# Performance work log

Hardware: AMD Instinct MI355X
Metric: run time of the kernel (lower is better)

The kernel has to match this reference:

```python
import jax, jax.numpy as jnp
import numpy as np

B, N, K = 8, 2048, 20
NC = 50
EPS = 1e-5
SLOPE = 0.2


def _knn(xt, k):
    # xt: [B, N, C]; negative squared euclidean distance, top-k (includes self)
    xx = jnp.sum(xt * xt, axis=-1)                      # [B, N]
    inner = jnp.einsum('bnc,bmc->bnm', xt, xt)          # [B, N, N]
    dist = 2.0 * inner - xx[:, :, None] - xx[:, None, :]
    return jax.lax.top_k(dist, k)[1]                    # [B, N, k] int32


def _edge_conv(xt, w, g, b, k):
    # xt: [B, N, C]; w: [O, 2C]; BatchNorm2d over (B, N, k) per out-channel.
    idx = _knn(xt, k)
    nbr = xt[jnp.arange(B)[:, None, None], idx]          # [B, N, k, C]
    ctr = jnp.broadcast_to(xt[:, :, None, :], nbr.shape)
    edge = jnp.concatenate([nbr - ctr, ctr], axis=-1)    # [B, N, k, 2C]
    h = jnp.einsum('bnkc,oc->bnko', edge, w)             # 1x1 conv, no bias
    mu = jnp.mean(h, axis=(0, 1, 2))
    var = jnp.var(h, axis=(0, 1, 2))
    h = (h - mu) / jnp.sqrt(var + EPS) * g + b
    h = jnp.where(h > 0, h, SLOPE * h)                   # LeakyReLU(0.2)
    return jnp.max(h, axis=2)                            # max over k -> [B, N, O]


def _bn1d(y, g, b):
    mu = jnp.mean(y, axis=0)
    var = jnp.var(y, axis=0)
    return (y - mu) / jnp.sqrt(var + EPS) * g + b


def setup_inputs() -> dict:
    key = jax.random.key(0)
    ks = jax.random.split(key, 20)

    def rn(k, shape, scale):
        return jax.random.normal(k, shape, dtype=jnp.float32) * scale

    d = {
        'x': rn(ks[0], (B * N, 3), 1.0),
        'pos': rn(ks[1], (B * N, 3), 1.0),
        'batch': jnp.repeat(jnp.arange(B, dtype=jnp.int64), N),
        'edge_index': jax.random.randint(ks[2], (2, B * N), 0, B * N, dtype=jnp.int64),
        # EdgeConv 1x1 conv weights [out, in], BN gamma/beta
        'w1': rn(ks[3], (64, 6), 0.3),   'g1': jnp.ones(64),  'b1': jnp.zeros(64),
        'w2': rn(ks[4], (64, 128), 0.1), 'g2': jnp.ones(64),  'b2': jnp.zeros(64),
        'w3': rn(ks[5], (128, 128), 0.1),'g3': jnp.ones(128), 'b3': jnp.zeros(128),
        'w4': rn(ks[6], (256, 256), 0.08),'g4': jnp.ones(256),'b4': jnp.zeros(256),
        # lin1: Linear(512,1024)+ReLU+BN1d(1024)
        'lw1': rn(ks[7], (512, 1024), 0.04), 'lb1': jnp.zeros(1024),
        'lg1': jnp.ones(1024), 'lbb1': jnp.zeros(1024),
        # mlp: [1024->256 +ReLU+BN] -> [256->128 +ReLU+BN] -> Lin(128, NC)
        'mw1': rn(ks[8], (1024, 256), 0.03), 'mb1': jnp.zeros(256),
        'mg1': jnp.ones(256), 'mbb1': jnp.zeros(256),
        'mw2': rn(ks[9], (256, 128), 0.06), 'mb2': jnp.zeros(128),
        'mg2': jnp.ones(128), 'mbb2': jnp.zeros(128),
        'hw': rn(ks[10], (128, NC), 0.09), 'hb': jnp.zeros(NC),
    }
    return d


def reference(x, pos, batch, edge_index,
              w1, g1, b1, w2, g2, b2, w3, g3, b3, w4, g4, b4,
              lw1, lb1, lg1, lbb1,
              mw1, mb1, mg1, mbb1, mw2, mb2, mg2, mbb2,
              hw, hb):
    # batch is sorted with N points per cloud -> static reshape
    xt = x.reshape(B, N, 3)
    x1 = _edge_conv(xt, w1, g1, b1, K)   # [B, N, 64]
    x2 = _edge_conv(x1, w2, g2, b2, K)   # [B, N, 64]
    x3 = _edge_conv(x2, w3, g3, b3, K)   # [B, N, 128]
    x4 = _edge_conv(x3, w4, g4, b4, K)   # [B, N, 256]
    cat = jnp.concatenate([x1, x2, x3, x4], axis=-1)  # [B, N, 512]
    h = cat.reshape(B * N, 512)
    h = _bn1d(jax.nn.relu(h @ lw1 + lb1), lg1, lbb1)
    h = _bn1d(jax.nn.relu(h @ mw1 + mb1), mg1, mbb1)   # dropout = identity (eval)
    h = _bn1d(jax.nn.relu(h @ mw2 + mb2), mg2, mbb2)
    logits = h @ hw + hb
    return jax.nn.log_softmax(logits, axis=1)
```

## Files before the change

### kernel.cpp

```cpp
#include <hip/hip_runtime.h>
#include <math.h>

#define NB 8
#define NP 2048
#define KNBR 20
#define NROWS (NB*NP)
#define SLOPEV 0.2f
#define EPSV 1e-5f

typedef short s8v __attribute__((ext_vector_type(8)));
typedef float f4v __attribute__((ext_vector_type(4)));
typedef double d4v __attribute__((ext_vector_type(4)));

__device__ __forceinline__ unsigned short f2bf(float f) {
    union { float f; unsigned u; } v; v.f = f;
    unsigned r = v.u + 0x7FFFu + ((v.u >> 16) & 1u);
    return (unsigned short)(r >> 16);
}

__global__ void mfma64_probe(int* __restrict__ tab)
{
    const int lane = threadIdx.x;
    d4v z = {0.0, 0.0, 0.0, 0.0};
    d4v pa = __builtin_amdgcn_mfma_f64_16x16x4f64((double)lane, 1.0, z, 0, 0, 0);
    d4v pb = __builtin_amdgcn_mfma_f64_16x16x4f64(1.0, (double)lane, z, 0, 0, 0);
    int famA = 1, famB = 1;
#pragma unroll
    for (int r = 0; r < 4; ++r) {
        int iv = (int)(pa[r] + 0.5);
        int row;
        if ((iv & 3) == 0 && iv >= 96) row = (iv - 96) >> 2;
        else { row = (iv - 6) >> 4; famA = 0; }
        int jv = (int)(pb[r] + 0.5);
        int col;
        if ((jv & 3) == 0 && jv >= 96) col = (jv - 96) >> 2;
        else { col = (jv - 6) >> 4; famB = 0; }
        tab[lane * 8 + r]     = row;
        tab[lane * 8 + 4 + r] = col;
    }
    tab[512 + lane] = famA;
    tab[576 + lane] = famB;
}

#define DK 16
__global__ __launch_bounds__(256, 2) void gemm64_dist(
    const double* __restrict__ A, int lda, int Kd,
    const double* __restrict__ xx, double* __restrict__ Cm, int batch0,
    const int* __restrict__ tab)
{
    __shared__ double As[DK][130];
    __shared__ double Bs[DK][66];
    const int tid = threadIdx.x;
    const int wave = tid >> 6, lane = tid & 63;
    const int quad = lane >> 4, l15 = lane & 15;
    const int bb = blockIdx.y;
    const int x  = blockIdx.x;
    int bi = (int)((sqrtf(4.0f * x + 1.0f) - 1.0f) * 0.5f);
    while (bi * (bi + 1) > x) --bi;
    while ((bi + 1) * (bi + 2) <= x) ++bi;
    const int bj = x - bi * (bi + 1);
    const int row0 = bi * 128, col0 = bj * 64;
    const double* Ab  = A + (size_t)(batch0 + bb) * NP * lda;
    double*       Cb  = Cm + (size_t)bb * NP * NP;
    const double* xxb = xx + (size_t)(batch0 + bb) * NP;

    int rT[4], cT[4];
#pragma unroll
    for (int r = 0; r < 4; ++r) { rT[r] = tab[lane * 8 + r]; cT[r] = tab[lane * 8 + 4 + r]; }
    const int famA = tab[512];
    const int famB = tab[576];
    const int am = famA ? l15 : (lane >> 2);
    const int ak = famA ? quad : (lane & 3);
    const int bn = famB ? l15 : (lane >> 2);
    const int bk = famB ? quad : (lane & 3);

    d4v acc[2][4];
#pragma unroll
    for (int mt = 0; mt < 2; ++mt)
#pragma unroll
        for (int nt = 0; nt < 4; ++nt) acc[mt][nt] = (d4v){0.0, 0.0, 0.0, 0.0};

    const int ma = tid >> 1, ka = (tid & 1) * 8;
    const int mb = tid >> 2, kb = (tid & 3) * 4;

    for (int kc = 0; kc < Kd; kc += DK) {
        const double* ap = Ab + (size_t)(row0 + ma) * lda + kc + ka;
#pragma unroll
        for (int i = 0; i < 8; ++i) {
            const int k2 = kc + ka + i;
            As[ka + i][ma] = (k2 < Kd) ? ap[i] : 0.0;
        }
        const double* bp = Ab + (size_t)(col0 + mb) * lda + kc + kb;
#pragma unroll
        for (int i = 0; i < 4; ++i) {
            const int k2 = kc + kb + i;
            Bs[kb + i][mb] = (k2 < Kd) ? bp[i] : 0.0;
        }
        __syncthreads();
#pragma unroll
        for (int kg = 0; kg < 4; ++kg) {
            const int k = kg * 4;
            double a0 = As[k + ak][wave * 32 + am];
            double a1 = As[k + ak][wave * 32 + 16 + am];
            double b0 = Bs[k + bk][bn];
            double b1 = Bs[k + bk][16 + bn];
            double b2 = Bs[k + bk][32 + bn];
            double b3 = Bs[k + bk][48 + bn];
            acc[0][0] = __builtin_amdgcn_mfma_f64_16x16x4f64(a0, b0, acc[0][0], 0, 0, 0);
            acc[0][1] = __builtin_amdgcn_mfma_f64_16x16x4f64(a0, b1, acc[0][1], 0, 0, 0);
            acc[0][2] = __builtin_amdgcn_mfma_f64_16x16x4f64(a0, b2, acc[0][2], 0, 0, 0);
            acc[0][3] = __builtin_amdgcn_mfma_f64_16x16x4f64(a0, b3, acc[0][3], 0, 0, 0);
            acc[1][0] = __builtin_amdgcn_mfma_f64_16x16x4f64(a1, b0, acc[1][0], 0, 0, 0);
            acc[1][1] = __builtin_amdgcn_mfma_f64_16x16x4f64(a1, b1, acc[1][1], 0, 0, 0);
            acc[1][2] = __builtin_amdgcn_mfma_f64_16x16x4f64(a1, b2, acc[1][2], 0, 0, 0);
            acc[1][3] = __builtin_amdgcn_mfma_f64_16x16x4f64(a1, b3, acc[1][3], 0, 0, 0);
        }
        __syncthreads();
    }

#pragma unroll
    for (int mt = 0; mt < 2; ++mt)
#pragma unroll
        for (int nt = 0; nt < 4; ++nt) {
#pragma unroll
            for (int rg = 0; rg < 4; ++rg) {
                const int r = row0 + wave * 32 + mt * 16 + rT[rg];
                const int c = col0 + nt * 16 + cT[rg];
                const double a2 = 2.0 * acc[mt][nt][rg];
                const double xr = xxb[r];
                const double xc = xxb[c];
                Cb[(size_t)r * NP + c] = (a2 - xr) - xc;
                Cb[(size_t)c * NP + r] = (a2 - xc) - xr;
            }
        }
}

__global__ __launch_bounds__(256, 2) void gemm64(
    const double* __restrict__ A, int lda,
    const double* __restrict__ Bm, int ldb,
    double* __restrict__ P, double* __restrict__ Q, int O, int Kd,
    const int* __restrict__ tab)
{
    __shared__ double As[DK][130];
    __shared__ double Bs[DK][66];
    const int tid = threadIdx.x;
    const int wave = tid >> 6, lane = tid & 63;
    const int quad = lane >> 4, l15 = lane & 15;
    const int row0 = blockIdx.y * 128, col0 = blockIdx.x * 64;

    int rT[4], cT[4];
#pragma unroll
    for (int r = 0; r < 4; ++r) { rT[r] = tab[lane * 8 + r]; cT[r] = tab[lane * 8 + 4 + r]; }
    const int famA = tab[512];
    const int famB = tab[576];
    const int am = famA ? l15 : (lane >> 2);
    const int ak = famA ? quad : (lane & 3);
    const int bn = famB ? l15 : (lane >> 2);
    const int bk = famB ? quad : (lane & 3);

    d4v acc[2][4];
#pragma unroll
    for (int mt = 0; mt < 2; ++mt)
#pragma unroll
        for (int nt = 0; nt < 4; ++nt) acc[mt][nt] = (d4v){0.0, 0.0, 0.0, 0.0};

    const int ma = tid >> 1, ka = (tid & 1) * 8;
    const int mb = tid >> 2, kb = (tid & 3) * 4;

    for (int kc = 0; kc < Kd; kc += DK) {
        const double* ap = A + (size_t)(row0 + ma) * lda + kc + ka;
#pragma unroll
        for (int i = 0; i < 8; ++i) {
            const int k2 = kc + ka + i;
            As[ka + i][ma] = (k2 < Kd) ? ap[i] : 0.0;
        }
        const double* bp = Bm + (size_t)(col0 + mb) * ldb + kc + kb;
#pragma unroll
        for (int i = 0; i < 4; ++i) {
            const int k2 = kc + kb + i;
            Bs[kb + i][mb] = (k2 < Kd) ? bp[i] : 0.0;
        }
        __syncthreads();
#pragma unroll
        for (int kg = 0; kg < 4; ++kg) {
            const int k = kg * 4;
            double a0 = As[k + ak][wave * 32 + am];
            double a1 = As[k + ak][wave * 32 + 16 + am];
            double b0 = Bs[k + bk][bn];
            double b1 = Bs[k + bk][16 + bn];
            double b2 = Bs[k + bk][32 + bn];
            double b3 = Bs[k + bk][48 + bn];
            acc[0][0] = __builtin_amdgcn_mfma_f64_16x16x4f64(a0, b0, acc[0][0], 0, 0, 0);
            acc[0][1] = __builtin_amdgcn_mfma_f64_16x16x4f64(a0, b1, acc[0][1], 0, 0, 0);
            acc[0][2] = __builtin_amdgcn_mfma_f64_16x16x4f64(a0, b2, acc[0][2], 0, 0, 0);
            acc[0][3] = __builtin_amdgcn_mfma_f64_16x16x4f64(a0, b3, acc[0][3], 0, 0, 0);
            acc[1][0] = __builtin_amdgcn_mfma_f64_16x16x4f64(a1, b0, acc[1][0], 0, 0, 0);
            acc[1][1] = __builtin_amdgcn_mfma_f64_16x16x4f64(a1, b1, acc[1][1], 0, 0, 0);
            acc[1][2] = __builtin_amdgcn_mfma_f64_16x16x4f64(a1, b2, acc[1][2], 0, 0, 0);
            acc[1][3] = __builtin_amdgcn_mfma_f64_16x16x4f64(a1, b3, acc[1][3], 0, 0, 0);
        }
        __syncthreads();
    }

    double* dst = (col0 < O) ? P : Q;
    const int cbase = (col0 < O) ? col0 : (col0 - O);
#pragma unroll
    for (int mt = 0; mt < 2; ++mt)
#pragma unroll
        for (int nt = 0; nt < 4; ++nt) {
#pragma unroll
            for (int rg = 0; rg < 4; ++rg) {
                const int r = row0 + wave * 32 + mt * 16 + rT[rg];
                const int c = cbase + nt * 16 + cT[rg];
                dst[(size_t)r * O + c] = acc[mt][nt][rg];
            }
        }
}

__global__ __launch_bounds__(256) void gemm_bf16(
    const float* __restrict__ A, int lda,
    const unsigned short* __restrict__ W,
    float* __restrict__ C, int ldc,
    int Kd,
    const float* __restrict__ bias,
    const float* __restrict__ a_ss)
{
    __shared__ unsigned short As[4][64][8];
    __shared__ unsigned short Bs[4][128][8];
    const int tid = threadIdx.x;
    const int wave = tid >> 6, lane = tid & 63;
    const int quad = lane >> 4, l15 = lane & 15;
    const int row0 = blockIdx.y * 64, col0 = blockIdx.x * 128;

    f4v acc[4][2];
#pragma unroll
    for (int mt = 0; mt < 4; ++mt)
#pragma unroll
        for (int nt = 0; nt < 2; ++nt) acc[mt][nt] = (f4v){0.f, 0.f, 0.f, 0.f};

    const int ar = tid >> 2, akc = tid & 3;
    const int br = tid >> 1, bkc = (tid & 1) * 2;

    for (int kc0 = 0; kc0 < Kd; kc0 += 32) {
        {
            const float* ap = A + (size_t)(row0 + ar) * lda + kc0 + akc * 8;
            float t0[8];
            *(float4*)&t0[0] = *(const float4*)ap;
            *(float4*)&t0[4] = *(const float4*)(ap + 4);
            if (a_ss) {
                const int kb = kc0 + akc * 8;
#pragma unroll
                for (int i = 0; i < 8; ++i)
                    t0[i] = fmaf(t0[i], a_ss[kb + i], a_ss[Kd + kb + i]);
            }
            unsigned short u[8];
#pragma unroll
            for (int i = 0; i < 8; ++i) u[i] = f2bf(t0[i]);
            *(uint4*)&As[akc][ar][0] = *(const uint4*)&u[0];
        }
        {
            const unsigned short* wp = W + (size_t)(col0 + br) * Kd + kc0 + bkc * 8;
            uint4 q0 = *(const uint4*)wp;
            uint4 q1 = *(const uint4*)(wp + 8);
            *(uint4*)&Bs[bkc][br][0]     = q0;
            *(uint4*)&Bs[bkc + 1][br][0] = q1;
        }
        __syncthreads();

        s8v a[4], b[2];
#pragma unroll
        for (int mt = 0; mt < 4; ++mt)
            a[mt] = *(const s8v*)&As[quad][mt * 16 + l15][0];
#pragma unroll
        for (int nt = 0; nt < 2; ++nt)
            b[nt] = *(const s8v*)&Bs[quad][wave * 32 + nt * 16 + l15][0];
#pragma unroll
        for (int mt = 0; mt < 4; ++mt)
#pragma unroll
            for (int nt = 0; nt < 2; ++nt)
                acc[mt][nt] = __builtin_amdgcn_mfma_f32_16x16x32_bf16(
                    a[mt], b[nt], acc[mt][nt], 0, 0, 0);
        __syncthreads();
    }

#pragma unroll
    for (int mt = 0; mt < 4; ++mt)
#pragma unroll
        for (int nt = 0; nt < 2; ++nt) {
            const int col = col0 + wave * 32 + nt * 16 + l15;
            const float bi = bias[col];
#pragma unroll
            for (int r = 0; r < 4; ++r) {
                const int row = row0 + mt * 16 + quad * 4 + r;
                float v = acc[mt][nt][r] + bi;
                v = fmaxf(v, 0.f);
                C[(size_t)row * ldc + col] = v;
            }
        }
}

#define GBK 16
__global__ __launch_bounds__(256, 2) void gemm_f32(
    const float* __restrict__ A, int lda,
    const float* __restrict__ Bm, int ldb,
    float* __restrict__ Cm, int ldc,
    int M, int Nn, int Kd, int mode,
    const float* __restrict__ bias,
    const float* __restrict__ a_ss)
{
    __shared__ float As[GBK][132];
    __shared__ float Bs[GBK][132];
    const int tid = threadIdx.x;
    const int tx = tid & 15, ty = tid >> 4;
    const int lin = blockIdx.y * gridDim.x + blockIdx.x;
    const int bx = lin / gridDim.y;
    const int by = lin - bx * gridDim.y;
    const int row0 = by * 128, col0 = bx * 128;
    float acc[8][8];
#pragma unroll
    for (int i = 0; i < 8; ++i)
#pragma unroll
        for (int j = 0; j < 8; ++j) acc[i][j] = 0.f;

    const int m  = tid >> 1;
    const int kk = (tid & 1) * 8;

    for (int kc = 0; kc < Kd; kc += GBK) {
        const int gc = col0 + m;
        const float* ap = A  + (size_t)(row0 + m) * lda + kc + kk;
        const float* bp = Bm + (size_t)gc * ldb + kc + kk;
#pragma unroll
        for (int i = 0; i < 8; ++i) {
            const int k2 = kc + kk + i;
            float v = 0.f;
            if (k2 < Kd) {
                v = ap[i];
                if (a_ss) v = fmaf(v, a_ss[k2], a_ss[Kd + k2]);
            }
            As[kk + i][m] = v;
        }
#pragma unroll
        for (int i = 0; i < 8; ++i) {
            const int k2 = kc + kk + i;
            float v = 0.f;
            if (gc < Nn && k2 < Kd) v = bp[i];
            Bs[kk + i][m] = v;
        }
        __syncthreads();
#pragma unroll
        for (int k = 0; k < GBK; ++k) {
            float4 a0 = *(const float4*)&As[k][ty * 4];
            float4 a1 = *(const float4*)&As[k][64 + ty * 4];
            float4 b0 = *(const float4*)&Bs[k][tx * 4];
            float4 b1 = *(const float4*)&Bs[k][64 + tx * 4];
            float a[8] = {a0.x, a0.y, a0.z, a0.w, a1.x, a1.y, a1.z, a1.w};
            float b[8] = {b0.x, b0.y, b0.z, b0.w, b1.x, b1.y, b1.z, b1.w};
#pragma unroll
            for (int i = 0; i < 8; ++i)
#pragma unroll
                for (int j = 0; j < 8; ++j) acc[i][j] = fmaf(a[i], b[j], acc[i][j]);
        }
        __syncthreads();
    }

#pragma unroll
    for (int i = 0; i < 8; ++i) {
        const int row = row0 + ty * 4 + (i & 3) + ((i >> 2) << 6);
        if (row >= M) continue;
#pragma unroll
        for (int h = 0; h < 2; ++h) {
            const int c0 = col0 + tx * 4 + (h << 6);
#pragma unroll
            for (int j = 0; j < 4; ++j) {
                const int col = c0 + j;
                if (col < Nn) {
                    float t = acc[i][h * 4 + j];
                    if (mode == 2)      t = fmaxf(t + bias[col], 0.f);
                    else if (mode == 3) t = t + bias[col];
                    Cm[(size_t)row * ldc + col] = t;
                }
            }
        }
    }
}

__global__ void f2d_kernel(const float* __restrict__ in, double* __restrict__ out, long n)
{
    long t = (long)blockIdx.x * 256 + threadIdx.x;
    if (t < n) out[t] = (double)in[t];
}
__global__ void d2f_kernel(const double* __restrict__ in, float* __restrict__ out, long n)
{
    long t = (long)blockIdx.x * 256 + threadIdx.x;
    if (t < n) out[t] = (float)in[t];
}

__global__ void xx_kernel_d(const double* __restrict__ F, int lda, int C,
                            double* __restrict__ xx)
{
    int r = blockIdx.x * 256 + threadIdx.x;
    if (r >= NROWS) return;
    const double* p = F + (long)r * lda;
    double s = 0.0;
    for (int c = 0; c < C; ++c) { double v = p[c]; s = fma(v, v, s); }
    xx[r] = s;
}

__global__ void wmod_kernel_d(const float* __restrict__ w, double* __restrict__ wm,
                              int O, int C)
{
    int t = blockIdx.x * 256 + threadIdx.x;
    if (t >= O * C) return;
    int o = t / C, c = t - o * C;
    double a = (double)w[o * 2 * C + c];
    double b = (double)w[o * 2 * C + C + c];
    wm[o * C + c] = a;
    wm[(O + o) * C + c] = b - a;
}

__global__ void transpose_kernel(const float* __restrict__ in, float* __restrict__ out,
                                 int R, int C)
{
    long t = (long)blockIdx.x * 256 + threadIdx.x;
    if (t >= (long)R * C) return;
    int r = (int)(t / C), c = (int)(t - (long)r * C);
    out[(long)c * R + r] = in[t];
}

__global__ void transpose_bf(const float* __restrict__ in, unsigned short* __restrict__ out,
                             int R, int C)
{
    long t = (long)blockIdx.x * 256 + threadIdx.x;
    if (t >= (long)R * C) return;
    int r = (int)(t / C), c = (int)(t - (long)r * C);
    out[(long)c * R + r] = f2bf(in[t]);
}

__global__ __launch_bounds__(256) void topk2(const double* __restrict__ D,
                                             int* __restrict__ out, int batch0)
{
    const int lane = threadIdx.x & 63;
    const int bb   = blockIdx.y;
    const int row  = blockIdx.x * 4 + (threadIdx.x >> 6);
    const double* rp = D + (size_t)bb * NP * NP + (size_t)row * NP;
    double v[32];
#pragma unroll
    for (int j = 0; j < 16; ++j) {
        double2 p = *(const double2*)&rp[j * 128 + lane * 2];
        v[2 * j] = p.x; v[2 * j + 1] = p.y;
    }
    double lbest = v[0];
    int    lidx  = lane * 2;
#pragma unroll
    for (int q = 1; q < 32; ++q) {
        const int col = ((q >> 1) << 7) + lane * 2 + (q & 1);
        if (v[q] > lbest) { lbest = v[q]; lidx = col; }
    }

    int* op = out + ((size_t)(batch0 + bb) * NP + row) * KNBR;
    const int jbase = (batch0 + bb) * NP;

    for (int it = 0; it < KNBR; ++it) {
        double best = lbest; int bidx = lidx;
#pragma unroll
        for (int off = 32; off >= 1; off >>= 1) {
            double ov = __shfl_xor(best, off, 64);
            int    oi = __shfl_xor(bidx, off, 64);
            if (ov > best || (ov == best && oi < bidx)) { best = ov; bidx = oi; }
        }
        if (lane == 0) op[it] = jbase + bidx;
        if (lane == ((bidx >> 1) & 63)) {
            const int q = (((bidx >> 7) << 1) | (bidx & 1));
#pragma unroll
            for (int qq = 0; qq < 32; ++qq) if (qq == q) v[qq] = -INFINITY;
            lbest = v[0]; lidx = lane * 2;
#pragma unroll
            for (int qq = 1; qq < 32; ++qq) {
                const int col = ((qq >> 1) << 7) + lane * 2 + (qq & 1);
                if (v[qq] > lbest) { lbest = v[qq]; lidx = col; }
            }
        }
    }
}

__global__ __launch_bounds__(256) void edge_gather(const double* __restrict__ P,
                                                   const double* __restrict__ Q,
                                                   const int* __restrict__ idx,
                                                   int O, int shiftO,
                                                   double* __restrict__ sums,
                                                   double* __restrict__ catOut, int ldo)
{
    const int tid = threadIdx.x;
    const int o = tid & (O - 1);
    const int q = tid >> shiftO;
    const int nsub = 256 >> shiftO;
    const int lin = blockIdx.x;
    const int r0 = (lin & 7) * NP + (lin >> 3) * 16;
    double s = 0.0, ss = 0.0;
    for (int r = r0 + q; r < r0 + 16; r += nsub) {
        const double qv = Q[(size_t)r * O + o];
        const int* ip = idx + r * KNBR;
        double m = -INFINITY;
        for (int k = 0; k < KNBR; ++k) {
            const int j = ip[k];
            const double v = P[(size_t)j * O + o] + qv;
            s += v; ss = fma(v, v, ss);
            m = fmax(m, v);
        }
        catOut[(size_t)r * ldo + o] = m;
    }
    __shared__ double red[256];
    red[tid] = s; __syncthreads();
    if (q == 0) for (int qq = 1; qq < nsub; ++qq) s += red[o + (qq << shiftO)];
    __syncthreads();
    red[tid] = ss; __syncthreads();
    if (q == 0) {
        for (int qq = 1; qq < nsub; ++qq) ss += red[o + (qq << shiftO)];
        atomicAdd(&sums[o], s);
        atomicAdd(&sums[O + o], ss);
    }
}

__global__ void bn_finalize_d(const double* __restrict__ sums,
                              const float* __restrict__ g, const float* __restrict__ b,
                              double* __restrict__ ss, int O, double invCnt)
{
    int o = blockIdx.x * 256 + threadIdx.x;
    if (o >= O) return;
    double mu  = sums[o] * invCnt;
    double var = sums[O + o] * invCnt - mu * mu;
    double is  = 1.0 / sqrt(var + 1e-5);
    double sc  = (double)g[o] * is;
    ss[o] = sc;
    ss[O + o] = (double)b[o] - mu * sc;
}

__global__ __launch_bounds__(256) void bn_apply(double* __restrict__ catOut, int ldo,
                                                const double* __restrict__ ssb,
                                                int O, int shiftO,
                                                const double* __restrict__ P,
                                                const double* __restrict__ Q,
                                                const int* __restrict__ idx)
{
    const int t = blockIdx.x * 256 + threadIdx.x;
    const int o = t & (O - 1);
    const int r = t >> shiftO;
    const double sc = ssb[o], sh = ssb[O + o];
    double v = catOut[(size_t)r * ldo + o];
    if (sc < 0.0) {
        const double qv = Q[(size_t)r * O + o];
        const int* ip = idx + r * KNBR;
        double m = INFINITY;
        for (int k = 0; k < KNBR; ++k)
            m = fmin(m, P[(size_t)ip[k] * O + o] + qv);
        v = m;
    }
    double u = fma(v, sc, sh);
    u = u > 0.0 ? u : 0.2 * u;
    catOut[(size_t)r * ldo + o] = u;
}

__global__ void col_stats(const float* __restrict__ Y, int ncol,
                          float* __restrict__ sums)
{
    int c  = blockIdx.x * 128 + threadIdx.x;
    int r0 = blockIdx.y * 256;
    float s = 0.f, ss = 0.f;
    for (int r = r0; r < r0 + 256; ++r) {
        float v = Y[(long)r * ncol + c];
        s += v; ss = fmaf(v, v, ss);
    }
    atomicAdd(&sums[c], s);
    atomicAdd(&sums[ncol + c], ss);
}

__global__ void bn_finalize_f(const float* __restrict__ sums,
                              const float* __restrict__ g, const float* __restrict__ b,
                              float* __restrict__ ss, int O, float invCnt)
{
    int o = blockIdx.x * 256 + threadIdx.x;
    if (o >= O) return;
    float mu  = sums[o] * invCnt;
    float var = sums[O + o] * invCnt - mu * mu;
    float is  = rsqrtf(var + EPSV);
    float sc  = g[o] * is;
    ss[o] = sc;
    ss[O + o] = b[o] - mu * sc;
}

__global__ __launch_bounds__(256) void log_softmax_kernel(float* __restrict__ Y)
{
    const int lane = threadIdx.x & 63;
    const int row  = blockIdx.x * 4 + (threadIdx.x >> 6);
    float v = -INFINITY;
    if (lane < 50) v = Y[(long)row * 50 + lane];
    float mx = v;
#pragma unroll
    for (int off = 32; off >= 1; off >>= 1) mx = fmaxf(mx, __shfl_xor(mx, off, 64));
    float e = (lane < 50) ? expf(v - mx) : 0.f;
    float s = e;
#pragma unroll
    for (int off = 32; off >= 1; off >>= 1) s += __shfl_xor(s, off, 64);
    float l = logf(s) + mx;
    if (lane < 50) Y[(long)row * 50 + lane] = v - l;
}

extern "C" void kernel_launch(void* const* d_in, const int* in_sizes, int n_in,
                              void* d_out, int out_size, void* d_ws, size_t ws_size,
                              hipStream_t stream)
{
    const float* x   = (const float*)d_in[0];
    const float* w[4]  = {(const float*)d_in[4], (const float*)d_in[7],
                          (const float*)d_in[10], (const float*)d_in[13]};
    const float* g[4]  = {(const float*)d_in[5], (const float*)d_in[8],
                          (const float*)d_in[11], (const float*)d_in[14]};
    const float* bb[4] = {(const float*)d_in[6], (const float*)d_in[9],
                          (const float*)d_in[12], (const float*)d_in[15]};
    const float* lw1 = (const float*)d_in[16]; const float* lb1 = (const float*)d_in[17];
    const float* lg1 = (const float*)d_in[18]; const float* lbb1 = (const float*)d_in[19];
    const float* mw1 = (const float*)d_in[20]; const float* mb1 = (const float*)d_in[21];
    const float* mg1 = (const float*)d_in[22]; const float* mbb1 = (const float*)d_in[23];
    const float* mw2 = (const float*)d_in[24]; const float* mb2 = (const float*)d_in[25];
    const float* mg2 = (const float*)d_in[26]; const float* mbb2 = (const float*)d_in[27];
    const float* hw  = (const float*)d_in[28]; const float* hb  = (const float*)d_in[29];
    float* out = (float*)d_out;

    char* base = (char*)d_ws;
    double* catD = (double*)base;
    char*  un    = base + 67108864;
    double* D    = (double*)un;
    double* Pb   = (double*)un;
    double* Qb   = (double*)(un + 33554432);
    float* cat32 = (float*)un;
    float* Y2    = (float*)(un + 33554432);
    float* Y3    = (float*)(un + 50331648);
    unsigned short* lw1Tb = (unsigned short*)(un + 58720256);
    unsigned short* mw1Tb = (unsigned short*)(un + 59768832);
    unsigned short* mw2Tb = (unsigned short*)(un + 60293120);
    float* hwT   = (float*)(un + 60358656);
    float* Y1    = (float*)base;
    char* tail = base + 2u * 67108864u;
    int*    idxb  = (int*)tail;
    double* xD    = (double*)(tail + 1310720);
    double* xxD   = (double*)(tail + 1703936);
    double* wmodD = (double*)(tail + 1835008);
    double* sumsD = (double*)(tail + 2359296);
    double* ssbD  = (double*)(tail + 2367488);
    float*  sumsF = (float*)(tail + 2375680);
    float*  ssbF  = (float*)(tail + 2383872);
    int*    mtab  = (int*)(tail + 2392064);

    mfma64_probe<<<1, 64, 0, stream>>>(mtab);

    f2d_kernel<<<(NROWS * 3 + 255) / 256, 256, 0, stream>>>(x, xD, (long)NROWS * 3);

    const double* Fin[4] = {xD, catD + 0, catD + 64, catD + 128};
    const int   ldaL[4] = {3, 512, 512, 512};
    const int   CL[4]   = {3, 64, 64, 128};
    const int   OL[4]   = {64, 64, 128, 256};
    const int   coff[4] = {0, 64, 128, 256};

    for (int l = 0; l < 4; ++l) {
        const double* F = Fin[l];
        const int lda = ldaL[l], C = CL[l], O = OL[l];
        const int shiftO = (O == 64) ? 6 : (O == 128) ? 7 : 8;

        wmod_kernel_d<<<(O * C + 255) / 256, 256, 0, stream>>>(w[l], wmodD, O, C);
        xx_kernel_d<<<NROWS / 256, 256, 0, stream>>>(F, lda, C, xxD);

        for (int p = 0; p < 4; ++p) {
            const int b0 = p * 2;
            gemm64_dist<<<dim3(272, 2), 256, 0, stream>>>(F, lda, C, xxD, D, b0, mtab);
            topk2<<<dim3(NP / 4, 2), 256, 0, stream>>>(D, idxb, b0);
        }

        gemm64<<<dim3((2 * O) / 64, NROWS / 128), 256, 0, stream>>>(
            F, lda, wmodD, C, Pb, Qb, O, C, mtab);

        hipMemsetAsync(sumsD, 0, 2 * O * sizeof(double), stream);
        edge_gather<<<NROWS / 16, 256, 0, stream>>>(Pb, Qb, idxb, O, shiftO, sumsD,
                                                    catD + coff[l], 512);
        bn_finalize_d<<<(O + 255) / 256, 256, 0, stream>>>(sumsD, g[l], bb[l], ssbD, O,
                                                           1.0 / ((double)NROWS * KNBR));
        bn_apply<<<(NROWS * O) / 256, 256, 0, stream>>>(catD + coff[l], 512, ssbD,
                                                        O, shiftO, Pb, Qb, idxb);
    }

    d2f_kernel<<<((long)NROWS * 512 + 255) / 256, 256, 0, stream>>>(catD, cat32, (long)NROWS * 512);

    transpose_bf<<<(512 * 1024 + 255) / 256, 256, 0, stream>>>(lw1, lw1Tb, 512, 1024);
    transpose_bf<<<(1024 * 256 + 255) / 256, 256, 0, stream>>>(mw1, mw1Tb, 1024, 256);
    transpose_bf<<<(256 * 128 + 255) / 256, 256, 0, stream>>>(mw2, mw2Tb, 256, 128);
    transpose_kernel<<<(128 * 50 + 255) / 256, 256, 0, stream>>>(hw, hwT, 128, 50);

    {
        gemm_bf16<<<dim3(1024 / 128, NROWS / 64), 256, 0, stream>>>(
            cat32, 512, lw1Tb, Y1, 1024, 512, lb1, nullptr);
        hipMemsetAsync(sumsF, 0, 2 * 1024 * sizeof(float), stream);
        col_stats<<<dim3(1024 / 128, 64), 128, 0, stream>>>(Y1, 1024, sumsF);
        bn_finalize_f<<<4, 256, 0, stream>>>(sumsF, lg1, lbb1, ssbF, 1024, 1.f / NROWS);
    }
    {
        gemm_bf16<<<dim3(256 / 128, NROWS / 64), 256, 0, stream>>>(
            Y1, 1024, mw1Tb, Y2, 256, 1024, mb1, ssbF);
        hipMemsetAsync(sumsF, 0, 2 * 256 * sizeof(float), stream);
        col_stats<<<dim3(256 / 128, 64), 128, 0, stream>>>(Y2, 256, sumsF);
        bn_finalize_f<<<1, 256, 0, stream>>>(sumsF, mg1, mbb1, ssbF, 256, 1.f / NROWS);
    }
    {
        gemm_bf16<<<dim3(128 / 128, NROWS / 64), 256, 0, stream>>>(
            Y2, 256, mw2Tb, Y3, 128, 256, mb2, ssbF);
        hipMemsetAsync(sumsF, 0, 2 * 128 * sizeof(float), stream);
        col_stats<<<dim3(1, 64), 128, 0, stream>>>(Y3, 128, sumsF);
        bn_finalize_f<<<1, 256, 0, stream>>>(sumsF, mg2, mbb2, ssbF, 128, 1.f / NROWS);
    }
    {
        dim3 gg(1, NROWS / 128);
        gemm_f32<<<gg, 256, 0, stream>>>(Y3, 128, hwT, 128, out, 50,
                                         NROWS, 50, 128, 3, hb, ssbF);
        log_softmax_kernel<<<NROWS / 4, 256, 0, stream>>>(out);
    }
}
```

Measured before the change: 2.225 ms.

## Fuse kNN distance GEMM with streaming top-k selection, drop full distance matrix

Replaces the per-batch-pair distance GEMM that wrote a full NxN double matrix, plus a separate top-k pass, with a fused kernel. Each block computes 64-row by 64-column distance tiles with f64 MFMA and keeps a running top-20 per row in registers, using a per-row threshold and bitmask so only candidates that beat the threshold get inserted. Each block covers half of the columns, and a small merge kernel combines the two half lists. This removes the large global write and re-read of the distance matrix, but the insertion step runs on only 64 threads per block and there are many block syncs.

After: 1.932 ms. 13.2% less time.

```diff
diff --git a/kernel.cpp b/kernel.cpp
--- a/kernel.cpp
+++ b/kernel.cpp
@@ -42,10 +42,171 @@
     tab[576 + lane] = famB;
 }
 
+template<int KD>
+__global__ __launch_bounds__(256, 2) void knn_fused2(
+    const double* __restrict__ F, int lda, int C,
+    const double* __restrict__ xx,
+    double* __restrict__ tmpv, int* __restrict__ tmpc,
+    const int* __restrict__ tab)
+{
+    constexpr int CH = (KD < 16) ? KD : 16;
+    __shared__ double Bs[CH][66];
+    __shared__ double Tile[64][65];
+    __shared__ double thr[64];
+    __shared__ unsigned msk[64][2];
+
+    const int tid = threadIdx.x;
+    const int wave = tid >> 6, lane = tid & 63;
+    const int bb    = blockIdx.z;
+    const int half  = blockIdx.y;
+    const int r0    = blockIdx.x * 64;
+    const int cbase = half * 1024;
+    const double* Fb  = F  + (size_t)bb * NP * lda;
+    const double* xxb = xx + (size_t)bb * NP;
+
+    int rT[4], cT[4];
+#pragma unroll
+    for (int r = 0; r < 4; ++r) { rT[r] = tab[lane * 8 + r]; cT[r] = tab[lane * 8 + 4 + r]; }
+    const int famA = tab[512];
+    const int famB = tab[576];
+    const int am = famA ? (lane & 15) : (lane >> 2);
+    const int ak = famA ? (lane >> 4) : (lane & 3);
+    const int bn = famB ? (lane & 15) : (lane >> 2);
+    const int bk = famB ? (lane >> 4) : (lane & 3);
+
+    const int arow = r0 + wave * 16 + am;
+    double areg[KD / 4];
+#pragma unroll
+    for (int j = 0; j < KD / 4; ++j) {
+        const int k = j * 4 + ak;
+        areg[j] = (k < C) ? Fb[(size_t)arow * lda + k] : 0.0;
+    }
+    double xr4[4];
+#pragma unroll
+    for (int rg = 0; rg < 4; ++rg)
+        xr4[rg] = xxb[r0 + wave * 16 + rT[rg]];
+
+    double kv[KNBR];
+    int    ki[KNBR];
+#pragma unroll
+    for (int q = 0; q < KNBR; ++q) { kv[q] = -INFINITY; ki[q] = 0; }
+    if (tid < 64) { thr[tid] = -INFINITY; msk[tid][0] = 0u; msk[tid][1] = 0u; }
+    __syncthreads();
+
+    for (int ct = 0; ct < 16; ++ct) {
+        const int c0 = cbase + ct * 64;
+        d4v acc[4];
+#pragma unroll
+        for (int nt = 0; nt < 4; ++nt) acc[nt] = (d4v){0.0, 0.0, 0.0, 0.0};
+
+#pragma unroll
+        for (int kc = 0; kc < KD; kc += CH) {
+            {
+                const int col = tid >> 2;
+                const int kb0 = (tid & 3) * (CH / 4);
+                const double* bp = Fb + (size_t)(c0 + col) * lda + kc + kb0;
+#pragma unroll
+                for (int i = 0; i < CH / 4; ++i) {
+                    const int k2 = kc + kb0 + i;
+                    Bs[kb0 + i][col] = (k2 < C) ? bp[i] : 0.0;
+                }
+            }
+            __syncthreads();
+#pragma unroll
+            for (int kg = 0; kg < CH / 4; ++kg) {
+                const double a  = areg[kc / 4 + kg];
+                const double b0 = Bs[kg * 4 + bk][bn];
+                const double b1 = Bs[kg * 4 + bk][16 + bn];
+                const double b2 = Bs[kg * 4 + bk][32 + bn];
+                const double b3 = Bs[kg * 4 + bk][48 + bn];
+                acc[0] = __builtin_amdgcn_mfma_f64_16x16x4f64(a, b0, acc[0], 0, 0, 0);
+                acc[1] = __builtin_amdgcn_mfma_f64_16x16x4f64(a, b1, acc[1], 0, 0, 0);
+                acc[2] = __builtin_amdgcn_mfma_f64_16x16x4f64(a, b2, acc[2], 0, 0, 0);
+                acc[3] = __builtin_amdgcn_mfma_f64_16x16x4f64(a, b3, acc[3], 0, 0, 0);
+            }
+            __syncthreads();
+        }
+
+#pragma unroll
+        for (int nt = 0; nt < 4; ++nt) {
+#pragma unroll
+            for (int rg = 0; rg < 4; ++rg) {
+                const int rloc = wave * 16 + rT[rg];
+                const int cloc = nt * 16 + cT[rg];
+                const double d = (2.0 * acc[nt][rg] - xr4[rg]) - xxb[c0 + cloc];
+                if (d > thr[rloc]) {
+                    Tile[rloc][cloc] = d;
+                    atomicOr(&msk[rloc][cloc >> 5], 1u << (cloc & 31));
+                }
+            }
+        }
+        __syncthreads();
+
+        if (tid < 64) {
+            bool changed = false;
+#pragma unroll
+            for (int w2 = 0; w2 < 2; ++w2) {
+                unsigned m = msk[tid][w2];
+                msk[tid][w2] = 0u;
+                while (m) {
+                    const int b = __ffs(m) - 1;
+                    m &= m - 1u;
+                    const double v = Tile[tid][w2 * 32 + b];
+                    if (v > kv[KNBR - 1]) {
+                        const int col = c0 + w2 * 32 + b;
+                        int pos = 0;
+#pragma unroll
+                        for (int q = 0; q < KNBR; ++q) pos += (kv[q] >= v) ? 1 : 0;
+#pragma unroll
+                        for (int q = KNBR - 1; q >= 0; --q) {
+                            if (q > pos)       { kv[q] = kv[q - 1]; ki[q] = ki[q - 1]; }
+                            else if (q == pos) { kv[q] = v;         ki[q] = col; }
+                        }
+                        changed = true;
+                    }
+                }
+            }
+            if (changed) thr[tid] = kv[KNBR - 1];
+        }
+        __syncthreads();
+    }
+
+    if (tid < 64) {
+        const size_t rowg = (size_t)bb * NP + r0 + tid;
+        double* vp = tmpv + (rowg * 2 + half) * KNBR;
+        int*    cp = tmpc + (rowg * 2 + half) * KNBR;
+#pragma unroll
+        for (int q = 0; q < KNBR; ++q) { vp[q] = kv[q]; cp[q] = ki[q]; }
+    }
+}
+
+__global__ void merge_topk(const double* __restrict__ tmpv,
+                           const int* __restrict__ tmpc,
+                           int* __restrict__ out)
+{
+    const int row = blockIdx.x * 256 + threadIdx.x;
+    if (row >= NROWS) return;
+    const double* va = tmpv + (size_t)row * 2 * KNBR;
+    const int*    ca = tmpc + (size_t)row * 2 * KNBR;
+    const double* vb = va + KNBR;
+    const int*    cb = ca + KNBR;
+    const int jbase = (row / NP) * NP;
+    int* op = out + (size_t)row * KNBR;
+    int ia = 0, ib = 0;
+#pragma unroll
+    for (int q = 0; q < KNBR; ++q) {
+        const double x = va[ia], y = vb[ib];
+        const bool takeA = (x > y) || (x == y && ca[ia] < cb[ib]);
+        if (takeA) { op[q] = jbase + ca[ia]; ++ia; }
+        else       { op[q] = jbase + cb[ib]; ++ib; }
+    }
+}
+
 #define DK 16
-__global__ __launch_bounds__(256, 2) void gemm64_dist(
-    const double* __restrict__ A, int lda, int Kd,
-    const double* __restrict__ xx, double* __restrict__ Cm, int batch0,
+__global__ __launch_bounds__(256, 2) void gemm64(
+    const double* __restrict__ A, int lda,
+    const double* __restrict__ Bm, int ldb,
+    double* __restrict__ P, double* __restrict__ Q, int O, int Kd,
     const int* __restrict__ tab)
 {
     __shared__ double As[DK][130];
@@ -53,16 +214,7 @@
     const int tid = threadIdx.x;
     const int wave = tid >> 6, lane = tid & 63;
     const int quad = lane >> 4, l15 = lane & 15;
-    const int bb = blockIdx.y;
-    const int x  = blockIdx.x;
-    int bi = (int)((sqrtf(4.0f * x + 1.0f) - 1.0f) * 0.5f);
-    while (bi * (bi + 1) > x) --bi;
-    while ((bi + 1) * (bi + 2) <= x) ++bi;
-    const int bj = x - bi * (bi + 1);
-    const int row0 = bi * 128, col0 = bj * 64;
-    const double* Ab  = A + (size_t)(batch0 + bb) * NP * lda;
-    double*       Cb  = Cm + (size_t)bb * NP * NP;
-    const double* xxb = xx + (size_t)(batch0 + bb) * NP;
+    const int row0 = blockIdx.y * 128, col0 = blockIdx.x * 64;
 
     int rT[4], cT[4];
 #pragma unroll
@@ -84,13 +236,13 @@
     const int mb = tid >> 2, kb = (tid & 3) * 4;
 
     for (int kc = 0; kc < Kd; kc += DK) {
-        const double* ap = Ab + (size_t)(row0 + ma) * lda + kc + ka;
+        const double* ap = A + (size_t)(row0 + ma) * lda + kc + ka;
 #pragma unroll
         for (int i = 0; i < 8; ++i) {
             const int k2 = kc + ka + i;
             As[ka + i][ma] = (k2 < Kd) ? ap[i] : 0.0;
         }
-        const double* bp = Ab + (size_t)(col0 + mb) * lda + kc + kb;
+        const double* bp = Bm + (size_t)(col0 + mb) * ldb + kc + kb;
 #pragma unroll
         for (int i = 0; i < 4; ++i) {
             const int k2 = kc + kb + i;
@@ -118,90 +270,6 @@
         __syncthreads();
     }
 
-#pragma unroll
-    for (int mt = 0; mt < 2; ++mt)
-#pragma unroll
-        for (int nt = 0; nt < 4; ++nt) {
-#pragma unroll
-            for (int rg = 0; rg < 4; ++rg) {
-                const int r = row0 + wave * 32 + mt * 16 + rT[rg];
-                const int c = col0 + nt * 16 + cT[rg];
-                const double a2 = 2.0 * acc[mt][nt][rg];
-                const double xr = xxb[r];
-                const double xc = xxb[c];
-                Cb[(size_t)r * NP + c] = (a2 - xr) - xc;
-                Cb[(size_t)c * NP + r] = (a2 - xc) - xr;
-            }
-        }
-}
-
-__global__ __launch_bounds__(256, 2) void gemm64(
-    const double* __restrict__ A, int lda,
-    const double* __restrict__ Bm, int ldb,
-    double* __restrict__ P, double* __restrict__ Q, int O, int Kd,
-    const int* __restrict__ tab)
-{
-    __shared__ double As[DK][130];
-    __shared__ double Bs[DK][66];
-    const int tid = threadIdx.x;
-    const int wave = tid >> 6, lane = tid & 63;
-    const int quad = lane >> 4, l15 = lane & 15;
-    const int row0 = blockIdx.y * 128, col0 = blockIdx.x * 64;
-
-    int rT[4], cT[4];
-#pragma unroll
-    for (int r = 0; r < 4; ++r) { rT[r] = tab[lane * 8 + r]; cT[r] = tab[lane * 8 + 4 + r]; }
-    const int famA = tab[512];
-    const int famB = tab[576];
-    const int am = famA ? l15 : (lane >> 2);
-    const int ak = famA ? quad : (lane & 3);
-    const int bn = famB ? l15 : (lane >> 2);
-    const int bk = famB ? quad : (lane & 3);
-
-    d4v acc[2][4];
-#pragma unroll
-    for (int mt = 0; mt < 2; ++mt)
-#pragma unroll
-        for (int nt = 0; nt < 4; ++nt) acc[mt][nt] = (d4v){0.0, 0.0, 0.0, 0.0};
-
-    const int ma = tid >> 1, ka = (tid & 1) * 8;
-    const int mb = tid >> 2, kb = (tid & 3) * 4;
-
-    for (int kc = 0; kc < Kd; kc += DK) {
-        const double* ap = A + (size_t)(row0 + ma) * lda + kc + ka;
-#pragma unroll
-        for (int i = 0; i < 8; ++i) {
-            const int k2 = kc + ka + i;
-            As[ka + i][ma] = (k2 < Kd) ? ap[i] : 0.0;
-        }
-        const double* bp = Bm + (size_t)(col0 + mb) * ldb + kc + kb;
-#pragma unroll
-        for (int i = 0; i < 4; ++i) {
-            const int k2 = kc + kb + i;
-            Bs[kb + i][mb] = (k2 < Kd) ? bp[i] : 0.0;
-        }
-        __syncthreads();
-#pragma unroll
-        for (int kg = 0; kg < 4; ++kg) {
-            const int k = kg * 4;
-            double a0 = As[k + ak][wave * 32 + am];
-            double a1 = As[k + ak][wave * 32 + 16 + am];
-            double b0 = Bs[k + bk][bn];
-            double b1 = Bs[k + bk][16 + bn];
-            double b2 = Bs[k + bk][32 + bn];
-            double b3 = Bs[k + bk][48 + bn];
-            acc[0][0] = __builtin_amdgcn_mfma_f64_16x16x4f64(a0, b0, acc[0][0], 0, 0, 0);
-            acc[0][1] = __builtin_amdgcn_mfma_f64_16x16x4f64(a0, b1, acc[0][1], 0, 0, 0);
-            acc[0][2] = __builtin_amdgcn_mfma_f64_16x16x4f64(a0, b2, acc[0][2], 0, 0, 0);
-            acc[0][3] = __builtin_amdgcn_mfma_f64_16x16x4f64(a0, b3, acc[0][3], 0, 0, 0);
-            acc[1][0] = __builtin_amdgcn_mfma_f64_16x16x4f64(a1, b0, acc[1][0], 0, 0, 0);
-            acc[1][1] = __builtin_amdgcn_mfma_f64_16x16x4f64(a1, b1, acc[1][1], 0, 0, 0);
-            acc[1][2] = __builtin_amdgcn_mfma_f64_16x16x4f64(a1, b2, acc[1][2], 0, 0, 0);
-            acc[1][3] = __builtin_amdgcn_mfma_f64_16x16x4f64(a1, b3, acc[1][3], 0, 0, 0);
-        }
-        __syncthreads();
-    }
-
     double* dst = (col0 < O) ? P : Q;
     const int cbase = (col0 < O) ? col0 : (col0 - O);
 #pragma unroll
@@ -434,53 +502,6 @@
     if (t >= (long)R * C) return;
     int r = (int)(t / C), c = (int)(t - (long)r * C);
     out[(long)c * R + r] = f2bf(in[t]);
-}
-
-__global__ __launch_bounds__(256) void topk2(const double* __restrict__ D,
-                                             int* __restrict__ out, int batch0)
-{
-    const int lane = threadIdx.x & 63;
-    const int bb   = blockIdx.y;
-    const int row  = blockIdx.x * 4 + (threadIdx.x >> 6);
-    const double* rp = D + (size_t)bb * NP * NP + (size_t)row * NP;
-    double v[32];
-#pragma unroll
-    for (int j = 0; j < 16; ++j) {
-        double2 p = *(const double2*)&rp[j * 128 + lane * 2];
-        v[2 * j] = p.x; v[2 * j + 1] = p.y;
-    }
-    double lbest = v[0];
-    int    lidx  = lane * 2;
-#pragma unroll
-    for (int q = 1; q < 32; ++q) {
-        const int col = ((q >> 1) << 7) + lane * 2 + (q & 1);
-        if (v[q] > lbest) { lbest = v[q]; lidx = col; }
-    }
-
-    int* op = out + ((size_t)(batch0 + bb) * NP + row) * KNBR;
-    const int jbase = (batch0 + bb) * NP;
-
-    for (int it = 0; it < KNBR; ++it) {
-        double best = lbest; int bidx = lidx;
-#pragma unroll
-        for (int off = 32; off >= 1; off >>= 1) {
-            double ov = __shfl_xor(best, off, 64);
-            int    oi = __shfl_xor(bidx, off, 64);
-            if (ov > best || (ov == best && oi < bidx)) { best = ov; bidx = oi; }
-        }
-        if (lane == 0) op[it] = jbase + bidx;
-        if (lane == ((bidx >> 1) & 63)) {
-            const int q = (((bidx >> 7) << 1) | (bidx & 1));
-#pragma unroll
-            for (int qq = 0; qq < 32; ++qq) if (qq == q) v[qq] = -INFINITY;
-            lbest = v[0]; lidx = lane * 2;
-#pragma unroll
-            for (int qq = 1; qq < 32; ++qq) {
-                const int col = ((qq >> 1) << 7) + lane * 2 + (qq & 1);
-                if (v[qq] > lbest) { lbest = v[qq]; lidx = col; }
-            }
-        }
-    }
 }
 
 __global__ __launch_bounds__(256) void edge_gather(const double* __restrict__ P,
@@ -628,7 +649,8 @@
     char* base = (char*)d_ws;
     double* catD = (double*)base;
     char*  un    = base + 67108864;
-    double* D    = (double*)un;
+    double* tmpv = (double*)un;
+    int*    tmpc = (int*)(un + 5242880);
     double* Pb   = (double*)un;
     double* Qb   = (double*)(un + 33554432);
     float* cat32 = (float*)un;
@@ -668,11 +690,14 @@
         wmod_kernel_d<<<(O * C + 255) / 256, 256, 0, stream>>>(w[l], wmodD, O, C);
         xx_kernel_d<<<NROWS / 256, 256, 0, stream>>>(F, lda, C, xxD);
 
-        for (int p = 0; p < 4; ++p) {
-            const int b0 = p * 2;
-            gemm64_dist<<<dim3(272, 2), 256, 0, stream>>>(F, lda, C, xxD, D, b0, mtab);
-            topk2<<<dim3(NP / 4, 2), 256, 0, stream>>>(D, idxb, b0);
-        }
+        dim3 kg(NP / 64, 2, NB);
+        if (C == 3)
+            knn_fused2<4><<<kg, 256, 0, stream>>>(F, lda, C, xxD, tmpv, tmpc, mtab);
+        else if (C == 64)
+            knn_fused2<64><<<kg, 256, 0, stream>>>(F, lda, C, xxD, tmpv, tmpc, mtab);
+        else
+            knn_fused2<128><<<kg, 256, 0, stream>>>(F, lda, C, xxD, tmpv, tmpc, mtab);
+        merge_topk<<<NROWS / 256, 256, 0, stream>>>(tmpv, tmpc, idxb);
 
         gemm64<<<dim3((2 * O) / 64, NROWS / 128), 256, 0, stream>>>(
             F, lda, wmodD, C, Pb, Qb, O, C, mtab);
```
